# Kernel tuning notes

Measured on AMD Instinct MI355X. Metric: run time of the kernel, lower is better.

Reference implementation:

```python
import jax, jax.numpy as jnp
import numpy as np
import math

B, S, E, H = 4, 1024, 1024, 16
DH = E // H  # head dim = 64


def setup_inputs() -> dict:
    key = jax.random.key(0)
    ks = jax.random.split(key, 10)
    w_scale = math.sqrt(2.0 / (E + 3 * E))  # xavier-ish
    return {
        "x_real": jax.random.normal(ks[0], (B, S, E), jnp.float32),
        "x_imag": jax.random.normal(ks[1], (B, S, E), jnp.float32),
        "w_packed_real": jax.random.normal(ks[2], (3 * E, E), jnp.float32) * w_scale,
        "w_packed_imag": jax.random.normal(ks[3], (3 * E, E), jnp.float32) * w_scale,
        "b_packed_real": jax.random.normal(ks[4], (1, 3 * E), jnp.float32) * 0.02,
        "b_packed_imag": jax.random.normal(ks[5], (1, 3 * E), jnp.float32) * 0.02,
        "w_out_real": jax.random.normal(ks[6], (E, E), jnp.float32) * w_scale,
        "w_out_imag": jax.random.normal(ks[7], (E, E), jnp.float32) * w_scale,
        "b_out_real": jax.random.normal(ks[8], (1, E), jnp.float32) * 0.02,
        "b_out_imag": jax.random.normal(ks[9], (1, E), jnp.float32) * 0.02,
    }


def _to_c(r, i):
    return jax.lax.complex(r, i)


def _cmha(x, w_packed, b_packed, w_out, b_out):
    # packed QKV projection: x [B,S,E] @ W^T [E,3E] + b
    qkv = jnp.matmul(x, w_packed.T) + b_packed  # [B,S,3E]
    q, k, v = jnp.split(qkv, 3, axis=-1)  # each [B,S,E]
    # split heads -> [B,H,S,DH]
    split = lambda t: t.reshape(B, S, H, DH).transpose(0, 2, 1, 3)
    q, k, v = split(q), split(k), split(v)
    scale = 1.0 / math.sqrt(DH)
    scores = jnp.einsum("bhqd,bhkd->bhqk", q, k) * scale  # complex [B,H,S,S]
    # complex softmax: softmax over real and imag parts independently
    attn = jax.lax.complex(jax.nn.softmax(scores.real, axis=-1),
                           jax.nn.softmax(scores.imag, axis=-1))
    out = jnp.einsum("bhqk,bhkd->bhqd", attn, v)  # [B,H,S,DH]
    out = out.transpose(0, 2, 1, 3).reshape(B, S, E)
    return jnp.matmul(out, w_out.T) + b_out  # [B,S,E] complex


def reference(x_real, x_imag, w_packed_real, w_packed_imag, b_packed_real,
              b_packed_imag, w_out_real, w_out_imag, b_out_real, b_out_imag):
    x = _to_c(x_real, x_imag)
    w_packed = _to_c(w_packed_real, w_packed_imag)
    b_packed = _to_c(b_packed_real, b_packed_imag)
    w_out = _to_c(w_out_real, w_out_imag)
    b_out = _to_c(b_out_real, b_out_imag)
    return _cmha(x, w_packed, b_packed, w_out, b_out)
```

## Files before the change

### kernel.cpp

```cpp
#include <hip/hip_runtime.h>


typedef _Float16 f16;
typedef _Float16 f16x8 __attribute__((ext_vector_type(8)));
typedef _Float16 f16x4 __attribute__((ext_vector_type(4)));
typedef float f32x4 __attribute__((ext_vector_type(4)));
typedef float f32x16 __attribute__((ext_vector_type(16)));

#define MFMA16(a, b, c) __builtin_amdgcn_mfma_f32_16x16x32_f16(a, b, c, 0, 0, 0)
#define MFMA32(a, b, c) __builtin_amdgcn_mfma_f32_32x32x16_f16(a, b, c, 0, 0, 0)

__device__ inline void load_lds16(const void* g, void* l) {
  __builtin_amdgcn_global_load_lds(
      (const __attribute__((address_space(1))) unsigned int*)g,
      (__attribute__((address_space(3))) unsigned int*)l, 16, 0, 0);
}

__device__ inline unsigned pkrtz(float a, float b) {
  auto t = __builtin_amdgcn_cvt_pkrtz(a, b);
  return __builtin_bit_cast(unsigned, t);
}


__global__ void pack_x_kernel(const float* __restrict__ xr, const float* __restrict__ xi,
                              f16* __restrict__ XC) {
  int i = blockIdx.x * 256 + threadIdx.x;
  if (i >= (4096 * 2048 / 4)) return;
  int idx = i * 4;
  int m = idx >> 11, k = idx & 2047;
  const float* src = (k < 1024) ? (xr + (size_t)m * 1024 + k) : (xi + (size_t)m * 1024 + k - 1024);
  float4 v = *(const float4*)src;
  f16x4 o = {(f16)v.x, (f16)v.y, (f16)v.z, (f16)v.w};
  *(f16x4*)(XC + idx) = o;
}

__global__ void pack_wqkv_kernel(const float* __restrict__ wr, const float* __restrict__ wi,
                                 f16* __restrict__ W) {
  int i = blockIdx.x * 256 + threadIdx.x;
  if (i >= (6144 * 2048 / 4)) return;
  int idx = i * 4;
  int n = idx >> 11, k = idx & 2047;
  const float* base;
  float sgn = 1.f;
  if (n < 3072) {
    if (k < 1024) base = wr + (size_t)n * 1024 + k;
    else { base = wi + (size_t)n * 1024 + k - 1024; sgn = -1.f; }
  } else {
    int n2 = n - 3072;
    if (k < 1024) base = wi + (size_t)n2 * 1024 + k;
    else base = wr + (size_t)n2 * 1024 + k - 1024;
  }
  float4 v = *(const float4*)base;
  f16x4 o = {(f16)(sgn * v.x), (f16)(sgn * v.y), (f16)(sgn * v.z), (f16)(sgn * v.w)};
  *(f16x4*)(W + idx) = o;
}

__global__ void pack_wout_kernel(const float* __restrict__ wor, const float* __restrict__ woi,
                                 f16* __restrict__ W) {
  int i = blockIdx.x * 256 + threadIdx.x;
  if (i >= (2048 * 2048 / 4)) return;
  int idx = i * 4;
  int n = idx >> 11, k = idx & 2047;
  const float* base;
  float sgn = 1.f;
  if (n < 1024) {
    if (k < 1024) base = wor + (size_t)n * 1024 + k;
    else { base = woi + (size_t)n * 1024 + k - 1024; sgn = -1.f; }
  } else {
    int n2 = n - 1024;
    if (k < 1024) base = woi + (size_t)n2 * 1024 + k;
    else base = wor + (size_t)n2 * 1024 + k - 1024;
  }
  float4 v = *(const float4*)base;
  f16x4 o = {(f16)(sgn * v.x), (f16)(sgn * v.y), (f16)(sgn * v.z), (f16)(sgn * v.w)};
  *(f16x4*)(W + idx) = o;
}

struct GemmParams {
  f16 *QC, *KCr, *KCi, *VCT;
  const float *bpr, *bpi;
  float* out;
  const float *bor, *boi;
  int out_complex;
};


__global__ __launch_bounds__(256, 3) void gemm1_kernel(const f16* __restrict__ A,
                                                       const f16* __restrict__ B,
                                                       GemmParams p) {
  const int K = 2048;
  __shared__ alignas(16) f16 sA[2][8192];
  __shared__ alignas(16) f16 sB[2][4096];
  const int tid = threadIdx.x;
  const int w = tid >> 6, l = tid & 63;
  const int lr = l & 15, lk = l >> 4;
  const int lin = blockIdx.x;
  const int xcd = lin & 7, idx = lin >> 3;
  const int mt = idx / 6, ntl = idx % 6;
  const int tm0 = mt * 256;
  const int tn0 = (xcd * 6 + ntl) * 128;
  const int wm = (w >> 1) * 128, wn = (w & 1) * 64;

  const int srow = tid >> 2;
  const int sk8 = ((tid & 3) ^ ((tid >> 3) & 3)) * 8;
  const f16* gA = A + (size_t)(tm0 + srow) * K + sk8;
  const f16* gB = B + (size_t)(tn0 + srow) * K + sk8;
  const int dst = w * 512;

#define STGA(buf, k0) do {                                                    \
    load_lds16(gA + (size_t)(k0), &sA[buf][dst]);                             \
    load_lds16(gA + (size_t)64 * K + (size_t)(k0), &sA[buf][2048 + dst]);     \
    load_lds16(gA + (size_t)128 * K + (size_t)(k0), &sA[buf][4096 + dst]);    \
    load_lds16(gA + (size_t)192 * K + (size_t)(k0), &sA[buf][6144 + dst]);    \
  } while (0)
#define STGB(buf, k0) do {                                                    \
    load_lds16(gB + (size_t)(k0), &sB[buf][dst]);                             \
    load_lds16(gB + (size_t)64 * K + (size_t)(k0), &sB[buf][2048 + dst]);     \
  } while (0)

  f32x4 acc[8][4] = {};

  STGA(0, 0);
  STGB(0, 0);
  asm volatile("s_waitcnt vmcnt(0)" ::: "memory");
  __syncthreads();

  const int ca = (lk ^ ((lr >> 1) & 3)) * 8;

  for (int t = 0; t < 64; ++t) {
    const int buf = t & 1;
    if (t < 63) {
      STGA(buf ^ 1, (t + 1) * 32);
      STGB(buf ^ 1, (t + 1) * 32);
    }
    const f16* pA = &sA[buf][0];
    const f16* pB = &sB[buf][0];
    f16x8 af[8], bf[4];
#pragma unroll
    for (int mi = 0; mi < 8; ++mi)
      af[mi] = *(const f16x8*)&pA[(wm + mi * 16 + lr) * 32 + ca];
#pragma unroll
    for (int nj = 0; nj < 4; ++nj)
      bf[nj] = *(const f16x8*)&pB[(wn + nj * 16 + lr) * 32 + ca];
#pragma unroll
    for (int mi = 0; mi < 8; ++mi)
#pragma unroll
      for (int nj = 0; nj < 4; ++nj)
        acc[mi][nj] = MFMA16(af[mi], bf[nj], acc[mi][nj]);
    asm volatile("s_waitcnt vmcnt(0)" ::: "memory");
    __syncthreads();
  }
#undef STGA
#undef STGB

#pragma unroll
  for (int mi = 0; mi < 8; ++mi)
#pragma unroll
    for (int nj = 0; nj < 4; ++nj) {
      int n = tn0 + wn + nj * 16 + lr;
      bool im = n >= 3072;
      int nn = im ? n - 3072 : n;
      float bias = im ? p.bpi[nn] : p.bpr[nn];
      int part = nn >> 10;
      int e = nn & 1023, h = e >> 6, dd = e & 63;
      int m0 = tm0 + wm + mi * 16 + lk * 4;
      int bb = m0 >> 10, s0 = m0 & 1023;
      size_t bh = (size_t)bb * 16 + h;
      if (part == 0) {
#pragma unroll
        for (int r = 0; r < 4; ++r)
          p.QC[(bh * 1024 + s0 + r) * 128 + (im ? 64 : 0) + dd] =
              (f16)((acc[mi][nj][r] + bias) * 0.125f);
      } else if (part == 1) {
#pragma unroll
        for (int r = 0; r < 4; ++r) {
          float v2 = acc[mi][nj][r] + bias;
          size_t o = (bh * 1024 + s0 + r) * 128;
          if (!im) { p.KCr[o + dd] = (f16)v2; p.KCi[o + 64 + dd] = (f16)v2; }
          else     { p.KCr[o + 64 + dd] = (f16)(-v2); p.KCi[o + dd] = (f16)v2; }
        }
      } else {
        f16x4 vv;
#pragma unroll
        for (int r = 0; r < 4; ++r) vv[r] = (f16)(acc[mi][nj][r] + bias);
        *(f16x4*)&p.VCT[((bh * 128 + (im ? 64 : 0) + dd)) * 1024 + s0] = vv;
      }
    }
}


__global__ __launch_bounds__(256) void gemm_out_kernel(const f16* __restrict__ A,
                                                       const f16* __restrict__ B,
                                                       GemmParams p) {
  const int K = 2048;
  __shared__ alignas(16) f16 sA[128 * 64];
  __shared__ alignas(16) f16 sB[128 * 64];
  const int tid = threadIdx.x;
  const int w = tid >> 6, l = tid & 63;
  const int lr = l & 15, lk = l >> 4;
  const int nwg = gridDim.x * gridDim.y;
  const int lin = blockIdx.y * gridDim.x + blockIdx.x;
  const int qq = nwg >> 3, rr = nwg & 7;
  const int xcd = lin & 7, off = lin >> 3;
  const int swz = (xcd < rr ? xcd * (qq + 1) : rr * (qq + 1) + (xcd - rr) * qq) + off;
  const int tm0 = (swz / gridDim.x) * 128;
  const int tn0 = (swz % gridDim.x) * 128;
  const int wm = (w >> 1) * 64, wn = (w & 1) * 64;

  f32x4 acc[4][4] = {};

  for (int k0 = 0; k0 < K; k0 += 64) {
#pragma unroll
    for (int i = 0; i < 4; ++i) {
      int slot = i * 256 + tid;
      int row = slot >> 3;
      int cg = (slot & 7) ^ (row & 7);
      load_lds16(A + (size_t)(tm0 + row) * K + k0 + cg * 8, &sA[(size_t)(i * 256 + (w << 6)) * 8]);
      load_lds16(B + (size_t)(tn0 + row) * K + k0 + cg * 8, &sB[(size_t)(i * 256 + (w << 6)) * 8]);
    }
    __syncthreads();
#pragma unroll
    for (int kk = 0; kk < 2; ++kk) {
      f16x8 af[4], bf[4];
#pragma unroll
      for (int t = 0; t < 4; ++t) {
        int rowA = wm + t * 16 + lr;
        af[t] = *(const f16x8*)&sA[rowA * 64 + ((kk * 4 + lk) ^ (rowA & 7)) * 8];
        int rowB = wn + t * 16 + lr;
        bf[t] = *(const f16x8*)&sB[rowB * 64 + ((kk * 4 + lk) ^ (rowB & 7)) * 8];
      }
#pragma unroll
      for (int mt = 0; mt < 4; ++mt)
#pragma unroll
        for (int nt = 0; nt < 4; ++nt) acc[mt][nt] = MFMA16(af[mt], bf[nt], acc[mt][nt]);
    }
    __syncthreads();
  }

#pragma unroll
  for (int mt = 0; mt < 4; ++mt)
#pragma unroll
    for (int nt = 0; nt < 4; ++nt)
#pragma unroll
      for (int r = 0; r < 4; ++r) {
        int m = tm0 + wm + mt * 16 + lk * 4 + r;
        int n = tn0 + wn + nt * 16 + lr;
        float val = acc[mt][nt][r];
        if (n < 1024) {
          float v2 = val + p.bor[n];
          if (p.out_complex) p.out[((size_t)m * 1024 + n) * 2] = v2;
          else p.out[(size_t)m * 1024 + n] = v2;
        } else {
          if (p.out_complex) p.out[((size_t)m * 1024 + n - 1024) * 2 + 1] = val + p.boi[n - 1024];
        }
      }
}


__global__ __launch_bounds__(256, 2) void attn_kernel(const f16* __restrict__ QC,
                                                      const f16* __restrict__ KCr,
                                                      const f16* __restrict__ KCi,
                                                      const f16* __restrict__ VCT,
                                                      f16* __restrict__ OC) {
  __shared__ alignas(16) f16 sKr[2][32 * 128];
  __shared__ alignas(16) f16 sKi[2][32 * 128];
  __shared__ alignas(16) f16 sV[2][128 * 32];
  const int tid = threadIdx.x;
  const int w = tid >> 6, l = tid & 63;
  const int lq = l & 31, hi = l >> 5;
  const int bid = blockIdx.x;
  const int xx = bid & 7, yy = bid >> 3;
  const int bh = xx + ((yy >> 3) << 3);
  const int qt = yy & 7;
  const int q0 = qt * 128 + w * 32;
  const f16* Qb = QC + (size_t)bh * 1024 * 128;
  const f16* Krb = KCr + (size_t)bh * 1024 * 128;
  const f16* Kib = KCi + (size_t)bh * 1024 * 128;
  const f16* Vb = VCT + (size_t)bh * 128 * 1024;

  f16x8 qf[8];
#pragma unroll
  for (int c = 0; c < 8; ++c)
    qf[c] = *(const f16x8*)&Qb[(size_t)(q0 + lq) * 128 + c * 16 + hi * 8];

  f32x16 accR[4] = {};
  f32x16 accI[4] = {};
  float m_r = -1e30f, l_r = 0.f, m_i = -1e30f, l_i = 0.f;

  const int sprow = tid >> 3;
  const int cK = (tid & 7) ^ ((tid >> 4) & 7);
  const f16* gKr = Krb + (size_t)(tid >> 4) * 128 + ((tid >> 3) & 1) * 64 + cK * 8;
  const f16* gKi = Kib + (size_t)(tid >> 4) * 128 + ((tid >> 3) & 1) * 64 + cK * 8;
  const int cV = (tid & 7) ^ (sprow & 7);
  const f16* gV = Vb + (size_t)(sprow * 2 + (cV >> 2)) * 1024 + (cV & 3) * 8;
  const int ldsW = w * 512;

#define STAGE(s, k0)                                                      \
  do {                                                                    \
    load_lds16(gKr + (size_t)(k0) * 128, &sKr[s][ldsW]);                  \
    load_lds16(gKr + (size_t)(k0) * 128 + 16 * 128, &sKr[s][2048 + ldsW]);\
    load_lds16(gKi + (size_t)(k0) * 128, &sKi[s][ldsW]);                  \
    load_lds16(gKi + (size_t)(k0) * 128 + 16 * 128, &sKi[s][2048 + ldsW]);\
    load_lds16(gV + (size_t)(k0), &sV[s][ldsW]);                          \
    load_lds16(gV + (size_t)64 * 1024 + (size_t)(k0), &sV[s][2048 + ldsW]);\
  } while (0)

  STAGE(0, 0);
  asm volatile("s_waitcnt vmcnt(0)" ::: "memory");
  __syncthreads();
  int cur = 0;

  for (int t = 0; t < 32; ++t) {
    if (t < 31) STAGE(cur ^ 1, (t + 1) * 32);

    f32x16 sr = {}, si = {};
    __builtin_amdgcn_s_setprio(1);
#pragma unroll
    for (int c = 0; c < 8; ++c) {
      int fc = c * 2 + hi;
      int prow = lq * 2 + (fc >> 3);
      int swzc = (fc & 7) ^ (lq & 7);
      f16x8 kr = *(const f16x8*)&sKr[cur][prow * 64 + swzc * 8];
      f16x8 ki = *(const f16x8*)&sKi[cur][prow * 64 + swzc * 8];
      sr = MFMA32(kr, qf[c], sr);
      si = MFMA32(ki, qf[c], si);
    }
    __builtin_amdgcn_s_setprio(0);

    f16x8 prf[2], pif[2];
#pragma unroll
    for (int part = 0; part < 2; ++part) {
      const f32x16& s = part ? si : sr;
      float& m = part ? m_i : m_r;
      float& lsum = part ? l_i : l_r;
      f32x16* acc = part ? accI : accR;
      float vm = s[0];
#pragma unroll
      for (int j = 1; j < 16; ++j) vm = fmaxf(vm, s[j]);
      vm = fmaxf(vm, __shfl_xor(vm, 32));
      if (__any(vm > m + 8.f)) {
        float mn = fmaxf(m, vm);
        float sc = __expf(m - mn);
        lsum *= sc;
#pragma unroll
        for (int a = 0; a < 4; ++a)
#pragma unroll
          for (int j = 0; j < 16; ++j) acc[a][j] *= sc;
        m = mn;
      }
      float p[16];
      float ls = 0.f;
#pragma unroll
      for (int j = 0; j < 16; ++j) { p[j] = __expf(s[j] - m); ls += p[j]; }
      lsum += ls;
      unsigned a0 = pkrtz(p[0], p[1]), b0 = pkrtz(p[4], p[5]);
      unsigned a1 = pkrtz(p[2], p[3]), b1 = pkrtz(p[6], p[7]);
      unsigned a2 = pkrtz(p[8], p[9]), b2 = pkrtz(p[12], p[13]);
      unsigned a3 = pkrtz(p[10], p[11]), b3 = pkrtz(p[14], p[15]);
      asm("v_permlane32_swap_b32 %0, %1" : "+v"(a0), "+v"(b0));
      asm("v_permlane32_swap_b32 %0, %1" : "+v"(a1), "+v"(b1));
      asm("v_permlane32_swap_b32 %0, %1" : "+v"(a2), "+v"(b2));
      asm("v_permlane32_swap_b32 %0, %1" : "+v"(a3), "+v"(b3));
      union { unsigned u[4]; f16x8 v; } f0, f1;
      f0.u[0] = a0; f0.u[1] = a1; f0.u[2] = b0; f0.u[3] = b1;
      f1.u[0] = a2; f1.u[1] = a3; f1.u[2] = b2; f1.u[3] = b3;
      if (part) { pif[0] = f0.v; pif[1] = f1.v; }
      else      { prf[0] = f0.v; prf[1] = f1.v; }
    }

    __builtin_amdgcn_s_setprio(1);
#pragma unroll
    for (int ft = 0; ft < 4; ++ft) {
#pragma unroll
      for (int ks = 0; ks < 2; ++ks) {
        int feat = ft * 32 + lq;
        int prow = feat >> 1;
        int swzc = (((feat & 1) * 4 + ks * 2 + hi) ^ (prow & 7));
        f16x8 vf = *(const f16x8*)&sV[cur][prow * 64 + swzc * 8];
        accR[ft] = MFMA32(vf, prf[ks], accR[ft]);
        accI[ft] = MFMA32(vf, pif[ks], accI[ft]);
      }
    }
    __builtin_amdgcn_s_setprio(0);

    asm volatile("s_waitcnt vmcnt(0)" ::: "memory");
    __syncthreads();
    cur ^= 1;
  }
#undef STAGE

  float lr = l_r + __shfl_xor(l_r, 32);
  float li = l_i + __shfl_xor(l_i, 32);
  float ilr = 1.f / lr, ili = 1.f / li;
  const int bb = bh >> 4, h = bh & 15;
  const int q = q0 + lq;
  f16* rowp = OC + ((size_t)bb * 1024 + q) * 2048 + h * 64;
#pragma unroll
  for (int tt = 0; tt < 2; ++tt) {
#pragma unroll
    for (int g = 0; g < 4; ++g) {
      int d0 = tt * 32 + g * 8 + hi * 4;
      f16x4 ov, oiv;
#pragma unroll
      for (int j = 0; j < 4; ++j) {
        int rg = g * 4 + j;
        float orv = accR[tt][rg] * ilr - accI[tt + 2][rg] * ili;
        float oivv = accR[tt + 2][rg] * ilr + accI[tt][rg] * ili;
        ov[j] = (f16)orv;
        oiv[j] = (f16)oivv;
      }
      *(f16x4*)(rowp + d0) = ov;
      *(f16x4*)(rowp + 1024 + d0) = oiv;
    }
  }
}


extern "C" void kernel_launch(void* const* d_in, const int* in_sizes, int n_in,
                              void* d_out, int out_size, void* d_ws, size_t ws_size,
                              hipStream_t stream) {
  const float* xr = (const float*)d_in[0];
  const float* xi = (const float*)d_in[1];
  const float* wpr = (const float*)d_in[2];
  const float* wpi = (const float*)d_in[3];
  const float* bpr = (const float*)d_in[4];
  const float* bpi = (const float*)d_in[5];
  const float* wor = (const float*)d_in[6];
  const float* woi = (const float*)d_in[7];
  const float* bor = (const float*)d_in[8];
  const float* boi = (const float*)d_in[9];

  f16* ws = (f16*)d_ws;
  f16* XC = ws;
  f16* WQKV = XC + 8388608;
  f16* QC = WQKV + 12582912;
  f16* KCr = QC + 8388608;
  f16* KCi = KCr + 8388608;
  f16* VCT = KCi + 8388608;
  f16* OC = VCT + 8388608;
  f16* WOUT = OC + 8388608;

  pack_x_kernel<<<8192, 256, 0, stream>>>(xr, xi, XC);
  pack_wqkv_kernel<<<12288, 256, 0, stream>>>(wpr, wpi, WQKV);
  pack_wout_kernel<<<4096, 256, 0, stream>>>(wor, woi, WOUT);

  GemmParams p1 = {};
  p1.QC = QC; p1.KCr = KCr; p1.KCi = KCi; p1.VCT = VCT;
  p1.bpr = bpr; p1.bpi = bpi;
  gemm1_kernel<<<768, 256, 0, stream>>>(XC, WQKV, p1);

  attn_kernel<<<512, 256, 0, stream>>>(QC, KCr, KCi, VCT, OC);

  GemmParams p2 = {};
  p2.out = (float*)d_out; p2.bor = bor; p2.boi = boi;
  p2.out_complex = (out_size == 8388608) ? 1 : 0;
  int ntilesN = p2.out_complex ? 16 : 8;
  gemm_out_kernel<<<dim3(ntilesN, 32), 256, 0, stream>>>(OC, WOUT, p2);
}
```

Before: 282.7 us.

## Use 3-multiply complex GEMM (Gauss trick) for QKV projection

Replaces the real-embedded 2x-wide complex GEMM for the QKV projection with a Gauss/Karatsuba-style three-product scheme (Ar*Br, Ai*Bi_neg, (Ar+Ai)*(Br-Bi_neg)), computing real and imaginary outputs from three MFMA accumulators. This halves the packed weight size and the pack_wqkv work and cuts MFMA count from four to three real products per complex product. The tile is shrunk to 128x64 with twice as many workgroups. The fp16 sums (Ar+Ai, Br-Bu) are formed in half precision, which adds rounding and overflow risk. Smaller tiles also lower data reuse per LDS load.

```diff
diff --git a/kernel.cpp b/kernel.cpp
--- a/kernel.cpp
+++ b/kernel.cpp
@@ -37,19 +37,13 @@
 __global__ void pack_wqkv_kernel(const float* __restrict__ wr, const float* __restrict__ wi,
                                  f16* __restrict__ W) {
   int i = blockIdx.x * 256 + threadIdx.x;
-  if (i >= (6144 * 2048 / 4)) return;
+  if (i >= (3072 * 2048 / 4)) return;
   int idx = i * 4;
   int n = idx >> 11, k = idx & 2047;
   const float* base;
   float sgn = 1.f;
-  if (n < 3072) {
-    if (k < 1024) base = wr + (size_t)n * 1024 + k;
-    else { base = wi + (size_t)n * 1024 + k - 1024; sgn = -1.f; }
-  } else {
-    int n2 = n - 3072;
-    if (k < 1024) base = wi + (size_t)n2 * 1024 + k;
-    else base = wr + (size_t)n2 * 1024 + k - 1024;
-  }
+  if (k < 1024) base = wr + (size_t)n * 1024 + k;
+  else { base = wi + (size_t)n * 1024 + k - 1024; sgn = -1.f; }
   float4 v = *(const float4*)base;
   f16x4 o = {(f16)(sgn * v.x), (f16)(sgn * v.y), (f16)(sgn * v.z), (f16)(sgn * v.w)};
   *(f16x4*)(W + idx) = o;
@@ -88,102 +82,117 @@
 __global__ __launch_bounds__(256, 3) void gemm1_kernel(const f16* __restrict__ A,
                                                        const f16* __restrict__ B,
                                                        GemmParams p) {
-  const int K = 2048;
-  __shared__ alignas(16) f16 sA[2][8192];
-  __shared__ alignas(16) f16 sB[2][4096];
+  const int KW = 2048;
+  __shared__ alignas(16) f16 sAr[2][4096];
+  __shared__ alignas(16) f16 sAi[2][4096];
+  __shared__ alignas(16) f16 sBr[2][2048];
+  __shared__ alignas(16) f16 sBu[2][2048];
   const int tid = threadIdx.x;
   const int w = tid >> 6, l = tid & 63;
   const int lr = l & 15, lk = l >> 4;
   const int lin = blockIdx.x;
   const int xcd = lin & 7, idx = lin >> 3;
   const int mt = idx / 6, ntl = idx % 6;
-  const int tm0 = mt * 256;
-  const int tn0 = (xcd * 6 + ntl) * 128;
-  const int wm = (w >> 1) * 128, wn = (w & 1) * 64;
+  const int tm0 = mt * 128;
+  const int tn0 = (xcd * 6 + ntl) * 64;
+  const int wm = (w >> 1) * 64, wn = (w & 1) * 32;
 
   const int srow = tid >> 2;
   const int sk8 = ((tid & 3) ^ ((tid >> 3) & 3)) * 8;
-  const f16* gA = A + (size_t)(tm0 + srow) * K + sk8;
-  const f16* gB = B + (size_t)(tn0 + srow) * K + sk8;
+  const f16* gAr = A + (size_t)(tm0 + srow) * KW + sk8;
+  const f16* gAi = A + (size_t)(tm0 + srow) * KW + 1024 + sk8;
+  const f16* gBr = B + (size_t)(tn0 + srow) * KW + sk8;
+  const f16* gBu = B + (size_t)(tn0 + srow) * KW + 1024 + sk8;
   const int dst = w * 512;
 
-#define STGA(buf, k0) do {                                                    \
-    load_lds16(gA + (size_t)(k0), &sA[buf][dst]);                             \
-    load_lds16(gA + (size_t)64 * K + (size_t)(k0), &sA[buf][2048 + dst]);     \
-    load_lds16(gA + (size_t)128 * K + (size_t)(k0), &sA[buf][4096 + dst]);    \
-    load_lds16(gA + (size_t)192 * K + (size_t)(k0), &sA[buf][6144 + dst]);    \
+#define STG(buf, k0) do {                                                  \
+    load_lds16(gAr + (size_t)(k0), &sAr[buf][dst]);                        \
+    load_lds16(gAr + (size_t)64 * KW + (size_t)(k0), &sAr[buf][2048 + dst]);\
+    load_lds16(gAi + (size_t)(k0), &sAi[buf][dst]);                        \
+    load_lds16(gAi + (size_t)64 * KW + (size_t)(k0), &sAi[buf][2048 + dst]);\
+    load_lds16(gBr + (size_t)(k0), &sBr[buf][dst]);                        \
+    load_lds16(gBu + (size_t)(k0), &sBu[buf][dst]);                        \
   } while (0)
-#define STGB(buf, k0) do {                                                    \
-    load_lds16(gB + (size_t)(k0), &sB[buf][dst]);                             \
-    load_lds16(gB + (size_t)64 * K + (size_t)(k0), &sB[buf][2048 + dst]);     \
-  } while (0)
-
-  f32x4 acc[8][4] = {};
-
-  STGA(0, 0);
-  STGB(0, 0);
+
+  f32x4 a1[4][2] = {};
+  f32x4 aU[4][2] = {};
+  f32x4 a3[4][2] = {};
+
+  STG(0, 0);
   asm volatile("s_waitcnt vmcnt(0)" ::: "memory");
   __syncthreads();
 
   const int ca = (lk ^ ((lr >> 1) & 3)) * 8;
 
-  for (int t = 0; t < 64; ++t) {
+  for (int t = 0; t < 32; ++t) {
     const int buf = t & 1;
-    if (t < 63) {
-      STGA(buf ^ 1, (t + 1) * 32);
-      STGB(buf ^ 1, (t + 1) * 32);
-    }
-    const f16* pA = &sA[buf][0];
-    const f16* pB = &sB[buf][0];
-    f16x8 af[8], bf[4];
-#pragma unroll
-    for (int mi = 0; mi < 8; ++mi)
-      af[mi] = *(const f16x8*)&pA[(wm + mi * 16 + lr) * 32 + ca];
-#pragma unroll
-    for (int nj = 0; nj < 4; ++nj)
-      bf[nj] = *(const f16x8*)&pB[(wn + nj * 16 + lr) * 32 + ca];
-#pragma unroll
-    for (int mi = 0; mi < 8; ++mi)
-#pragma unroll
-      for (int nj = 0; nj < 4; ++nj)
-        acc[mi][nj] = MFMA16(af[mi], bf[nj], acc[mi][nj]);
+    if (t < 31) STG(buf ^ 1, (t + 1) * 32);
+    f16x8 ar[4], ai[4], br[2], bu[2];
+#pragma unroll
+    for (int mi = 0; mi < 4; ++mi) {
+      ar[mi] = *(const f16x8*)&sAr[buf][(wm + mi * 16 + lr) * 32 + ca];
+      ai[mi] = *(const f16x8*)&sAi[buf][(wm + mi * 16 + lr) * 32 + ca];
+    }
+#pragma unroll
+    for (int nj = 0; nj < 2; ++nj) {
+      br[nj] = *(const f16x8*)&sBr[buf][(wn + nj * 16 + lr) * 32 + ca];
+      bu[nj] = *(const f16x8*)&sBu[buf][(wn + nj * 16 + lr) * 32 + ca];
+    }
+#pragma unroll
+    for (int mi = 0; mi < 4; ++mi)
+#pragma unroll
+      for (int nj = 0; nj < 2; ++nj) {
+        a1[mi][nj] = MFMA16(ar[mi], br[nj], a1[mi][nj]);
+        aU[mi][nj] = MFMA16(ai[mi], bu[nj], aU[mi][nj]);
+      }
+#pragma unroll
+    for (int mi = 0; mi < 4; ++mi) ar[mi] = ar[mi] + ai[mi];
+#pragma unroll
+    for (int nj = 0; nj < 2; ++nj) br[nj] = br[nj] - bu[nj];
+#pragma unroll
+    for (int mi = 0; mi < 4; ++mi)
+#pragma unroll
+      for (int nj = 0; nj < 2; ++nj)
+        a3[mi][nj] = MFMA16(ar[mi], br[nj], a3[mi][nj]);
     asm volatile("s_waitcnt vmcnt(0)" ::: "memory");
     __syncthreads();
   }
-#undef STGA
-#undef STGB
-
-#pragma unroll
-  for (int mi = 0; mi < 8; ++mi)
-#pragma unroll
-    for (int nj = 0; nj < 4; ++nj) {
+#undef STG
+
+#pragma unroll
+  for (int mi = 0; mi < 4; ++mi)
+#pragma unroll
+    for (int nj = 0; nj < 2; ++nj) {
       int n = tn0 + wn + nj * 16 + lr;
-      bool im = n >= 3072;
-      int nn = im ? n - 3072 : n;
-      float bias = im ? p.bpi[nn] : p.bpr[nn];
-      int part = nn >> 10;
-      int e = nn & 1023, h = e >> 6, dd = e & 63;
+      float br_ = p.bpr[n], bi_ = p.bpi[n];
+      int part = n >> 10;
+      int e = n & 1023, h = e >> 6, dd = e & 63;
       int m0 = tm0 + wm + mi * 16 + lk * 4;
       int bb = m0 >> 10, s0 = m0 & 1023;
       size_t bh = (size_t)bb * 16 + h;
+      f32x4 re = a1[mi][nj] + aU[mi][nj];
+      f32x4 im = a3[mi][nj] - a1[mi][nj] + aU[mi][nj];
       if (part == 0) {
 #pragma unroll
-        for (int r = 0; r < 4; ++r)
-          p.QC[(bh * 1024 + s0 + r) * 128 + (im ? 64 : 0) + dd] =
-              (f16)((acc[mi][nj][r] + bias) * 0.125f);
+        for (int r = 0; r < 4; ++r) {
+          size_t o = (bh * 1024 + s0 + r) * 128;
+          p.QC[o + dd] = (f16)((re[r] + br_) * 0.125f);
+          p.QC[o + 64 + dd] = (f16)((im[r] + bi_) * 0.125f);
+        }
       } else if (part == 1) {
 #pragma unroll
         for (int r = 0; r < 4; ++r) {
-          float v2 = acc[mi][nj][r] + bias;
+          float vr = re[r] + br_, vi = im[r] + bi_;
           size_t o = (bh * 1024 + s0 + r) * 128;
-          if (!im) { p.KCr[o + dd] = (f16)v2; p.KCi[o + 64 + dd] = (f16)v2; }
-          else     { p.KCr[o + 64 + dd] = (f16)(-v2); p.KCi[o + dd] = (f16)v2; }
+          p.KCr[o + dd] = (f16)vr; p.KCr[o + 64 + dd] = (f16)(-vi);
+          p.KCi[o + dd] = (f16)vi; p.KCi[o + 64 + dd] = (f16)vr;
         }
       } else {
-        f16x4 vv;
-#pragma unroll
-        for (int r = 0; r < 4; ++r) vv[r] = (f16)(acc[mi][nj][r] + bias);
-        *(f16x4*)&p.VCT[((bh * 128 + (im ? 64 : 0) + dd)) * 1024 + s0] = vv;
+        f16x4 vvr, vvi;
+#pragma unroll
+        for (int r = 0; r < 4; ++r) { vvr[r] = (f16)(re[r] + br_); vvi[r] = (f16)(im[r] + bi_); }
+        *(f16x4*)&p.VCT[((bh * 128 + dd)) * 1024 + s0] = vvr;
+        *(f16x4*)&p.VCT[((bh * 128 + 64 + dd)) * 1024 + s0] = vvi;
       }
     }
 }
@@ -433,7 +442,7 @@
   f16* ws = (f16*)d_ws;
   f16* XC = ws;
   f16* WQKV = XC + 8388608;
-  f16* QC = WQKV + 12582912;
+  f16* QC = WQKV + 6291456;
   f16* KCr = QC + 8388608;
   f16* KCi = KCr + 8388608;
   f16* VCT = KCi + 8388608;
@@ -441,13 +450,13 @@
   f16* WOUT = OC + 8388608;
 
   pack_x_kernel<<<8192, 256, 0, stream>>>(xr, xi, XC);
-  pack_wqkv_kernel<<<12288, 256, 0, stream>>>(wpr, wpi, WQKV);
+  pack_wqkv_kernel<<<6144, 256, 0, stream>>>(wpr, wpi, WQKV);
   pack_wout_kernel<<<4096, 256, 0, stream>>>(wor, woi, WOUT);
 
   GemmParams p1 = {};
   p1.QC = QC; p1.KCr = KCr; p1.KCi = KCi; p1.VCT = VCT;
   p1.bpr = bpr; p1.bpi = bpi;
-  gemm1_kernel<<<768, 256, 0, stream>>>(XC, WQKV, p1);
+  gemm1_kernel<<<1536, 256, 0, stream>>>(XC, WQKV, p1);
 
   attn_kernel<<<512, 256, 0, stream>>>(QC, KCr, KCi, VCT, OC);
 
```

After: 263.3 us. 6.9% less time.
